# Kernel tuning notes

Measured on AMD Instinct MI355X. Metric: run time of the kernel, lower is better.

Reference implementation:

```python
import jax, jax.numpy as jnp
import numpy as np


def setup_inputs() -> dict:
    key = jax.random.key(0)
    ks = jax.random.split(key, 7)
    N, C, sy, sx = 1024, 384, 7, 7
    Dm, Dc = 64, 64
    Dg = C + Dm + Dc  # 512, must match f_t_global
    return {
        "f_t_global": jax.random.normal(ks[0], (N, Dg), dtype=jnp.float32),
        "x_t_local": jax.random.normal(ks[1], (N, C, sy, sx), dtype=jnp.float32),
        "x_t_prev_local": jax.random.normal(ks[2], (N, C, sy, sx), dtype=jnp.float32),
        "m_t": jax.random.normal(ks[3], (N, Dm), dtype=jnp.float32),
        "m_t_prev": jax.random.normal(ks[4], (N, Dm), dtype=jnp.float32),
        "c_t": jax.random.normal(ks[5], (N, Dc), dtype=jnp.float32),
        "c_t_prev": jax.random.normal(ks[6], (N, Dc), dtype=jnp.float32),
    }


def _join(loc, m, c):
    # loc: [S, N, C]; m: [N, Dm]; c: [N, Dc] -> [S, N, C+Dm+Dc]
    S, N, _ = loc.shape
    mc = jnp.concatenate([m, c], axis=-1)  # [N, Dm+Dc]
    mc = jnp.broadcast_to(mc[None], (S, N, mc.shape[-1]))
    return jnp.concatenate([loc, mc], axis=-1)


def _mean_ce_diag(logits):
    # logits: [S, N, N]; labels = arange(N) for every s -> mean over s of CE
    logp = jax.nn.log_softmax(logits, axis=-1)
    diag = jnp.diagonal(logp, axis1=1, axis2=2)  # [S, N]
    return -jnp.mean(diag)  # mean over N (per-step CE) and over S (the /(sx*sy))


def reference(f_t_global, x_t_local, x_t_prev_local, m_t, m_t_prev, c_t, c_t_prev):
    N, C, sy, sx = x_t_prev_local.shape
    S = sy * sx
    # [N,C,sy,sx] -> [S,N,C] (spatial locations batched)
    prev = x_t_prev_local.reshape(N, C, S).transpose(2, 0, 1)
    cur = x_t_local.reshape(N, C, S).transpose(2, 0, 1)
    pos = _join(prev, m_t_prev, c_t_prev)   # [S, N, D]
    # loss1: global features vs per-location previous positives
    logits1 = jnp.einsum('id,sjd->sij', f_t_global, pos)  # [S, N, N]
    loss1 = _mean_ce_diag(logits1)
    # loss2: per-location current predictions vs previous positives
    pred2 = _join(cur, m_t, c_t)            # [S, N, D]
    logits2 = jnp.einsum('sid,sjd->sij', pred2, pos)
    loss2 = _mean_ce_diag(logits2)
    loss = loss1 + loss2
    return (loss, x_t_prev_local, x_t_local)
```

## Files before the change

kernel.cpp:

```cpp
#include <hip/hip_runtime.h>
#include <hip/hip_bf16.h>

typedef __attribute__((ext_vector_type(8))) __bf16 bf16x8;
typedef __attribute__((ext_vector_type(4))) float  f32x4;

#define SDIM 49
#define NDIM 1024
#define CDIM 384
#define DDIM 512
#define DMC  64
#define SCALE (1.0f/(SDIM*NDIM))
#define SLOT4 32768
#define CHUNK 24576

__device__ __forceinline__ void gload16(const void* g, void* l) {
    __builtin_amdgcn_global_load_lds((const __attribute__((address_space(1))) void*)g,
                                     (__attribute__((address_space(3))) void*)l, 16, 0, 0);
}

__global__ __launch_bounds__(512) void front_kernel(
    const float* __restrict__ xp, const float* __restrict__ mp,
    const float* __restrict__ cp, __hip_bfloat16* __restrict__ Km,
    const float* __restrict__ x,  const float* __restrict__ mt,
    const float* __restrict__ ct, __hip_bfloat16* __restrict__ Qm,
    const float* __restrict__ f,  __hip_bfloat16* __restrict__ Fm,
    float* __restrict__ out0)
{
    const int bid = blockIdx.x;
    const int tid = threadIdx.x;

    if (tid < 256) {
        const int i = bid * 256 + tid;
        Fm[i] = __float2bfloat16(f[i]);
    }
    if (bid == 0 && tid == 0) out0[0] = 0.0f;

    const bool kside = (bid < 1024);
    const int j = kside ? bid : (bid - 1024);
    const float* xloc = kside ? xp : x;
    const float* mv   = kside ? mp : mt;
    const float* cv   = kside ? cp : ct;
    __hip_bfloat16* dst = kside ? Km : Qm;

    const int d = tid;
    float vals[SDIM];
    if (d < CDIM) {
        const float* p = xloc + ((size_t)j * CDIM + d) * SDIM;
        #pragma unroll
        for (int s = 0; s < SDIM; ++s) vals[s] = p[s];
    } else if (d < CDIM + DMC) {
        float v = mv[j * DMC + (d - CDIM)];
        #pragma unroll
        for (int s = 0; s < SDIM; ++s) vals[s] = v;
    } else {
        float v = cv[j * DMC + (d - CDIM - DMC)];
        #pragma unroll
        for (int s = 0; s < SDIM; ++s) vals[s] = v;
    }
    #pragma unroll
    for (int s = 0; s < SDIM; ++s)
        dst[((size_t)s * NDIM + j) * DDIM + d] = __float2bfloat16(vals[s]);
}

__global__ __launch_bounds__(512, 2) void loss_kernel(
    const __hip_bfloat16* __restrict__ Fm,
    const __hip_bfloat16* __restrict__ Km,
    const __hip_bfloat16* __restrict__ Qm,
    const float* __restrict__ xp,
    const float* __restrict__ xq,
    float* __restrict__ outv,
    float2* __restrict__ part,
    float* __restrict__ out)
{
    extern __shared__ __attribute__((aligned(16))) char sm[];

    const int bid = blockIdx.x;
    const int xcd = bid & 7;
    const int jj  = bid >> 3;
    const int g0  = 196 * xcd;
    const int gend = g0 + 196;

    const int tid  = threadIdx.x;
    const int lane = tid & 63;
    const int w    = tid >> 6;
    const int l15  = lane & 15;
    const int l4   = lane >> 4;
    const int wk   = w >> 2;
    const int wq   = w & 3;

    const int srow = tid >> 2;
    const int jcol = (((tid & 3) - ((tid >> 3) & 3)) & 3) << 4;

    const unsigned off   = (unsigned)(((l4 + (l15 >> 1)) & 3) << 4);
    const unsigned abase = (unsigned)((wk * 128 + l15) * 64);
    const unsigned bbase = 16384u + (unsigned)((wq * 64 + l15) * 64);

    auto APtr = [&](int g) -> const char* {
        const int s = g >> 5, kb = (g >> 3) & 3;
        return (const char*)Km + ((size_t)s * NDIM + (size_t)kb * 256) * 1024;
    };
    auto BPtr = [&](int g) -> const char* {
        const int s = g >> 5, qb = g & 7;
        return (qb < 4)
            ? ((const char*)Fm + (size_t)qb * 256 * 1024)
            : ((const char*)Qm + ((size_t)s * NDIM + (size_t)(qb - 4) * 256) * 1024);
    };
    auto stage4 = [&](const char* A, const char* B, int ko, char* slot) {
        #pragma unroll
        for (int c = 0; c < 2; ++c) {
            gload16(A + (size_t)(c * 128 + srow) * 1024 + ko + jcol,
                    slot + c * 8192 + tid * 16);
            gload16(B + (size_t)(c * 128 + srow) * 1024 + ko + jcol,
                    slot + 16384 + c * 8192 + tid * 16);
        }
    };

    f32x4 acc[8][4];
    bf16x8 afr[8], bfr[4];

    #define READ12() do {                                                     \
        _Pragma("unroll")                                                     \
        for (int a = 0; a < 8; ++a)                                           \
            afr[a] = *(const bf16x8*)(sb_ + abase + a * 1024u + off);         \
        _Pragma("unroll")                                                     \
        for (int b = 0; b < 4; ++b)                                           \
            bfr[b] = *(const bf16x8*)(sb_ + bbase + b * 1024u + off);         \
    } while (0)

    #define MFMA32() do {                                                     \
        _Pragma("unroll")                                                     \
        for (int a = 0; a < 8; ++a)                                           \
            _Pragma("unroll")                                                 \
            for (int b = 0; b < 4; ++b)                                       \
                acc[a][b] = __builtin_amdgcn_mfma_f32_16x16x32_bf16(          \
                    afr[a], bfr[b], acc[a][b], 0, 0, 0);                      \
    } while (0)

    {
        const char* A0 = APtr(g0 + jj);
        const char* B0 = BPtr(g0 + jj);
        stage4(A0, B0, 0,   sm);
        stage4(A0, B0, 64,  sm + SLOT4);
        stage4(A0, B0, 128, sm + 2 * SLOT4);
        asm volatile("s_waitcnt vmcnt(0)" ::: "memory");
    }

    for (int g = g0 + jj; g < gend; g += 32) {
        const char* Ag = APtr(g);
        const char* Bg = BPtr(g);
        const bool hasNext = (g + 32) < gend;
        const char* An = hasNext ? APtr(g + 32) : Ag;
        const char* Bn = hasNext ? BPtr(g + 32) : Bg;

        #pragma unroll
        for (int a = 0; a < 8; ++a)
            #pragma unroll
            for (int b = 0; b < 4; ++b) acc[a][b] = f32x4{0.f, 0.f, 0.f, 0.f};

        #pragma unroll
        for (int t = 0; t < 16; ++t) {
            const char* sb_ = sm + (size_t)(t & 3) * SLOT4;
            char* ns_ = sm + (size_t)((t + 3) & 3) * SLOT4;

            if (t == 15)      asm volatile("s_waitcnt vmcnt(0)" ::: "memory");
            else if (t == 14) asm volatile("s_waitcnt vmcnt(4)" ::: "memory");
            else if (t >= 3)  asm volatile("s_waitcnt vmcnt(8)" ::: "memory");
            __builtin_amdgcn_s_barrier();

            if (t <= 12) {
                stage4(Ag, Bg, (t + 3) * 64, ns_);
            } else if (hasNext) {
                stage4(An, Bn, (t - 13) * 64, ns_);
            }
            __builtin_amdgcn_sched_barrier(0);

            READ12();
            __builtin_amdgcn_s_setprio(1); MFMA32(); __builtin_amdgcn_s_setprio(0);
        }

        const int s  = g >> 5;
        const int kb = (g >> 3) & 3;
        const int qb = g & 7;

        const float* csrc = (g < 784) ? (xp + (size_t)g * CHUNK)
                                      : (xq + (size_t)(g - 784) * CHUNK);
        float* cdst = outv + (size_t)g * CHUNK;
        f32x4 cbuf[12];
        #pragma unroll
        for (int i = 0; i < 12; ++i)
            cbuf[i] = *(const f32x4*)(csrc + tid * 4 + i * 2048);

        float q_m[4], q_s[4];
        #pragma unroll
        for (int b = 0; b < 4; ++b) {
            float m = -3.0e38f;
            #pragma unroll
            for (int a = 0; a < 8; ++a)
                #pragma unroll
                for (int r = 0; r < 4; ++r) m = fmaxf(m, acc[a][b][r]);
            float ss = 0.0f;
            #pragma unroll
            for (int a = 0; a < 8; ++a)
                #pragma unroll
                for (int r = 0; r < 4; ++r) ss += __expf(acc[a][b][r] - m);
            #pragma unroll
            for (int off2 = 16; off2 <= 32; off2 <<= 1) {
                float mo = __shfl_xor(m, off2, 64);
                float so = __shfl_xor(ss, off2, 64);
                float nm = fmaxf(m, mo);
                ss = ss * __expf(m - nm) + so * __expf(mo - nm);
                m = nm;
            }
            q_m[b] = m; q_s[b] = ss;
        }

        if (kb == (qb & 3) && (wq >> 1) == wk) {
            float d = 0.0f;
            const bool lok = (((lane >> 2) & 3) == l4);
            if (wq & 1) {
                #pragma unroll
                for (int b = 0; b < 4; ++b)
                    #pragma unroll
                    for (int r = 0; r < 4; ++r)
                        if (lok && r == (lane & 3)) d += acc[4 + b][b][r];
            } else {
                #pragma unroll
                for (int b = 0; b < 4; ++b)
                    #pragma unroll
                    for (int r = 0; r < 4; ++r)
                        if (lok && r == (lane & 3)) d += acc[b][b][r];
            }
            #pragma unroll
            for (int off2 = 1; off2 < 64; off2 <<= 1) d += __shfl_xor(d, off2, 64);
            if (lane == 0) atomicAdd(out, -d * SCALE);
        }

        asm volatile("s_waitcnt vmcnt(0)" ::: "memory");
        #pragma unroll
        for (int i = 0; i < 12; ++i)
            *(f32x4*)(cdst + tid * 4 + i * 2048) = cbuf[i];

        if (lane < 16) {
            const size_t rowb = (size_t)s * 2048 + (size_t)qb * 256 + wq * 64 + lane;
            #pragma unroll
            for (int b = 0; b < 4; ++b)
                part[(rowb + b * 16) * 8 + kb * 2 + wk] = make_float2(q_m[b], q_s[b]);
        }
    }
    #undef READ12
    #undef MFMA32
}

__global__ __launch_bounds__(256) void reduce_kernel(
    const float2* __restrict__ part, float* __restrict__ out)
{
    const int row = blockIdx.x * 256 + threadIdx.x;
    const float2* p = part + (size_t)row * 8;
    float m = -3.0e38f;
    float2 q[8];
    #pragma unroll
    for (int i = 0; i < 8; ++i) { q[i] = p[i]; m = fmaxf(m, q[i].x); }
    float ssum = 0.0f;
    #pragma unroll
    for (int i = 0; i < 8; ++i) ssum += q[i].y * __expf(q[i].x - m);
    float v = m + __logf(ssum);
    #pragma unroll
    for (int off = 1; off < 64; off <<= 1) v += __shfl_xor(v, off, 64);
    __shared__ float red[4];
    const int lane = threadIdx.x & 63, w = threadIdx.x >> 6;
    if (lane == 0) red[w] = v;
    __syncthreads();
    if (threadIdx.x == 0)
        atomicAdd(out, (red[0] + red[1] + red[2] + red[3]) * SCALE);
}

extern "C" void kernel_launch(void* const* d_in, const int* in_sizes, int n_in,
                              void* d_out, int out_size, void* d_ws, size_t ws_size,
                              hipStream_t stream)
{
    (void)in_sizes; (void)n_in; (void)out_size; (void)ws_size;
    const float* f  = (const float*)d_in[0];
    const float* x  = (const float*)d_in[1];
    const float* xp = (const float*)d_in[2];
    const float* mt = (const float*)d_in[3];
    const float* mp = (const float*)d_in[4];
    const float* ct = (const float*)d_in[5];
    const float* cp = (const float*)d_in[6];
    float* out = (float*)d_out;

    char* ws = (char*)d_ws;
    const size_t packBytes = (size_t)SDIM * NDIM * DDIM * 2;
    __hip_bfloat16* Km = (__hip_bfloat16*)ws;
    __hip_bfloat16* Qm = (__hip_bfloat16*)(ws + packBytes);
    __hip_bfloat16* Fm = (__hip_bfloat16*)(ws + 2 * packBytes);
    float2* part = (float2*)(ws + 2 * packBytes + (size_t)NDIM * DDIM * 2);

    front_kernel<<<2048, 512, 0, stream>>>(xp, mp, cp, Km, x, mt, ct, Qm, f, Fm, out);
    loss_kernel<<<256, 512, 4 * SLOT4, stream>>>(Fm, Km, Qm, xp, x, out + 1, part, out);
    reduce_kernel<<<392, 256, 0, stream>>>(part, out);
}
```

Before: 208.7 us.

## Halve loss-kernel tile width, use triple-buffered LDS and double the grid

The loss GEMM tile shrinks from 256x256 to 256x128 per work item. Each block now stages A and B through three LDS slots instead of four, and the grid grows from 256 to 512 blocks with launch bounds asking for 4 blocks per CU. The partial softmax stats grow to 16 per row, and the reduce kernel is updated to merge them. The aim is higher occupancy and better latency hiding from smaller register and LDS footprints, at the cost of less data reuse per tile and more partial-stat traffic.

```diff
diff --git a/kernel.cpp b/kernel.cpp
--- a/kernel.cpp
+++ b/kernel.cpp
@@ -10,8 +10,8 @@
 #define DDIM 512
 #define DMC  64
 #define SCALE (1.0f/(SDIM*NDIM))
-#define SLOT4 32768
-#define CHUNK 24576
+#define SLOT3 24576
+#define CHUNK 12288
 
 __device__ __forceinline__ void gload16(const void* g, void* l) {
     __builtin_amdgcn_global_load_lds((const __attribute__((address_space(1))) void*)g,
@@ -62,7 +62,7 @@
         dst[((size_t)s * NDIM + j) * DDIM + d] = __float2bfloat16(vals[s]);
 }
 
-__global__ __launch_bounds__(512, 2) void loss_kernel(
+__global__ __launch_bounds__(512, 4) void loss_kernel(
     const __hip_bfloat16* __restrict__ Fm,
     const __hip_bfloat16* __restrict__ Km,
     const __hip_bfloat16* __restrict__ Qm,
@@ -77,117 +77,113 @@
     const int bid = blockIdx.x;
     const int xcd = bid & 7;
     const int jj  = bid >> 3;
-    const int g0  = 196 * xcd;
-    const int gend = g0 + 196;
 
     const int tid  = threadIdx.x;
     const int lane = tid & 63;
     const int w    = tid >> 6;
     const int l15  = lane & 15;
     const int l4   = lane >> 4;
-    const int wk   = w >> 2;
-    const int wq   = w & 3;
-
-    const int srow = tid >> 2;
+    const int wk   = w >> 1;
+    const int wq   = w & 1;
+
     const int jcol = (((tid & 3) - ((tid >> 3) & 3)) & 3) << 4;
 
     const unsigned off   = (unsigned)(((l4 + (l15 >> 1)) & 3) << 4);
-    const unsigned abase = (unsigned)((wk * 128 + l15) * 64);
+    const unsigned abase = (unsigned)((wk * 64 + l15) * 64);
     const unsigned bbase = 16384u + (unsigned)((wq * 64 + l15) * 64);
 
     auto APtr = [&](int g) -> const char* {
-        const int s = g >> 5, kb = (g >> 3) & 3;
+        const int s = g >> 6, kb = (g >> 4) & 3;
         return (const char*)Km + ((size_t)s * NDIM + (size_t)kb * 256) * 1024;
     };
     auto BPtr = [&](int g) -> const char* {
-        const int s = g >> 5, qb = g & 7;
-        return (qb < 4)
-            ? ((const char*)Fm + (size_t)qb * 256 * 1024)
-            : ((const char*)Qm + ((size_t)s * NDIM + (size_t)(qb - 4) * 256) * 1024);
+        const int s = g >> 6, qb = g & 15;
+        return (qb < 8)
+            ? ((const char*)Fm + (size_t)qb * 128 * 1024)
+            : ((const char*)Qm + ((size_t)s * NDIM + (size_t)(qb - 8) * 128) * 1024);
     };
-    auto stage4 = [&](const char* A, const char* B, int ko, char* slot) {
-        #pragma unroll
-        for (int c = 0; c < 2; ++c) {
-            gload16(A + (size_t)(c * 128 + srow) * 1024 + ko + jcol,
-                    slot + c * 8192 + tid * 16);
-            gload16(B + (size_t)(c * 128 + srow) * 1024 + ko + jcol,
-                    slot + 16384 + c * 8192 + tid * 16);
-        }
+    auto stage3 = [&](const char* A, const char* B, int ko, char* slot) {
+        const int r = tid >> 2;
+        gload16(A + (size_t)r * 1024 + ko + jcol,        slot + tid * 16);
+        gload16(A + (size_t)(128 + r) * 1024 + ko + jcol, slot + 8192 + tid * 16);
+        gload16(B + (size_t)r * 1024 + ko + jcol,        slot + 16384 + tid * 16);
     };
 
-    f32x4 acc[8][4];
-    bf16x8 afr[8], bfr[4];
-
-    #define READ12() do {                                                     \
+    f32x4 acc[4][4];
+    bf16x8 afr[4], bfr[4];
+
+    #define READ8() do {                                                      \
         _Pragma("unroll")                                                     \
-        for (int a = 0; a < 8; ++a)                                           \
+        for (int a = 0; a < 4; ++a)                                           \
             afr[a] = *(const bf16x8*)(sb_ + abase + a * 1024u + off);         \
         _Pragma("unroll")                                                     \
         for (int b = 0; b < 4; ++b)                                           \
             bfr[b] = *(const bf16x8*)(sb_ + bbase + b * 1024u + off);         \
     } while (0)
 
-    #define MFMA32() do {                                                     \
+    #define MFMA16() do {                                                     \
         _Pragma("unroll")                                                     \
-        for (int a = 0; a < 8; ++a)                                           \
+        for (int a = 0; a < 4; ++a)                                           \
             _Pragma("unroll")                                                 \
             for (int b = 0; b < 4; ++b)                                       \
                 acc[a][b] = __builtin_amdgcn_mfma_f32_16x16x32_bf16(          \
                     afr[a], bfr[b], acc[a][b], 0, 0, 0);                      \
     } while (0)
 
+    int cs = 0;
+
     {
-        const char* A0 = APtr(g0 + jj);
-        const char* B0 = BPtr(g0 + jj);
-        stage4(A0, B0, 0,   sm);
-        stage4(A0, B0, 64,  sm + SLOT4);
-        stage4(A0, B0, 128, sm + 2 * SLOT4);
-        asm volatile("s_waitcnt vmcnt(0)" ::: "memory");
-    }
-
-    for (int g = g0 + jj; g < gend; g += 32) {
+        const int gg = 392 * xcd + jj;
+        stage3(APtr(gg), BPtr(gg), 0,  sm);
+        stage3(APtr(gg), BPtr(gg), 64, sm + SLOT3);
+    }
+
+    for (int l = jj; l < 392; l += 64) {
+        const int g = 392 * xcd + l;
         const char* Ag = APtr(g);
         const char* Bg = BPtr(g);
-        const bool hasNext = (g + 32) < gend;
-        const char* An = hasNext ? APtr(g + 32) : Ag;
-        const char* Bn = hasNext ? BPtr(g + 32) : Bg;
-
-        #pragma unroll
-        for (int a = 0; a < 8; ++a)
+        const bool hasNext = (l + 64) < 392;
+        const int gn = hasNext ? (g + 64) : g;
+        const char* An = APtr(gn);
+        const char* Bn = BPtr(gn);
+
+        #pragma unroll
+        for (int a = 0; a < 4; ++a)
             #pragma unroll
             for (int b = 0; b < 4; ++b) acc[a][b] = f32x4{0.f, 0.f, 0.f, 0.f};
 
         #pragma unroll
         for (int t = 0; t < 16; ++t) {
-            const char* sb_ = sm + (size_t)(t & 3) * SLOT4;
-            char* ns_ = sm + (size_t)((t + 3) & 3) * SLOT4;
-
-            if (t == 15)      asm volatile("s_waitcnt vmcnt(0)" ::: "memory");
-            else if (t == 14) asm volatile("s_waitcnt vmcnt(4)" ::: "memory");
-            else if (t >= 3)  asm volatile("s_waitcnt vmcnt(8)" ::: "memory");
+            const char* sb_ = sm + (size_t)cs * SLOT3;
+            int ps = cs + 2; if (ps >= 3) ps -= 3;
+            char* ns_ = sm + (size_t)ps * SLOT3;
+
+            if (t == 15 && !hasNext) asm volatile("s_waitcnt vmcnt(0)" ::: "memory");
+            else                     asm volatile("s_waitcnt vmcnt(3)" ::: "memory");
             __builtin_amdgcn_s_barrier();
 
-            if (t <= 12) {
-                stage4(Ag, Bg, (t + 3) * 64, ns_);
+            if (t < 14) {
+                stage3(Ag, Bg, (t + 2) * 64, ns_);
             } else if (hasNext) {
-                stage4(An, Bn, (t - 13) * 64, ns_);
+                stage3(An, Bn, (t - 14) * 64, ns_);
             }
             __builtin_amdgcn_sched_barrier(0);
 
-            READ12();
-            __builtin_amdgcn_s_setprio(1); MFMA32(); __builtin_amdgcn_s_setprio(0);
-        }
-
-        const int s  = g >> 5;
-        const int kb = (g >> 3) & 3;
-        const int qb = g & 7;
-
-        const float* csrc = (g < 784) ? (xp + (size_t)g * CHUNK)
-                                      : (xq + (size_t)(g - 784) * CHUNK);
+            READ8();
+            __builtin_amdgcn_s_setprio(1); MFMA16(); __builtin_amdgcn_s_setprio(0);
+            cs = (cs == 2) ? 0 : cs + 1;
+        }
+
+        const int s  = g >> 6;
+        const int kb = (g >> 4) & 3;
+        const int qb = g & 15;
+
+        const float* csrc = (g < 1568) ? (xp + (size_t)g * CHUNK)
+                                       : (xq + (size_t)(g - 1568) * CHUNK);
         float* cdst = outv + (size_t)g * CHUNK;
-        f32x4 cbuf[12];
-        #pragma unroll
-        for (int i = 0; i < 12; ++i)
+        f32x4 cbuf[6];
+        #pragma unroll
+        for (int i = 0; i < 6; ++i)
             cbuf[i] = *(const f32x4*)(csrc + tid * 4 + i * 2048);
 
         float q_m[4], q_s[4];
@@ -195,12 +191,12 @@
         for (int b = 0; b < 4; ++b) {
             float m = -3.0e38f;
             #pragma unroll
-            for (int a = 0; a < 8; ++a)
+            for (int a = 0; a < 4; ++a)
                 #pragma unroll
                 for (int r = 0; r < 4; ++r) m = fmaxf(m, acc[a][b][r]);
             float ss = 0.0f;
             #pragma unroll
-            for (int a = 0; a < 8; ++a)
+            for (int a = 0; a < 4; ++a)
                 #pragma unroll
                 for (int r = 0; r < 4; ++r) ss += __expf(acc[a][b][r] - m);
             #pragma unroll
@@ -214,22 +210,14 @@
             q_m[b] = m; q_s[b] = ss;
         }
 
-        if (kb == (qb & 3) && (wq >> 1) == wk) {
+        if (kb == ((qb & 7) >> 1) && wk == ((qb & 7) & 1) * 2 + wq) {
             float d = 0.0f;
-            const bool lok = (((lane >> 2) & 3) == l4);
-            if (wq & 1) {
+            const bool lok = ((l15 >> 2) == l4);
+            #pragma unroll
+            for (int b = 0; b < 4; ++b)
                 #pragma unroll
-                for (int b = 0; b < 4; ++b)
-                    #pragma unroll
-                    for (int r = 0; r < 4; ++r)
-                        if (lok && r == (lane & 3)) d += acc[4 + b][b][r];
-            } else {
-                #pragma unroll
-                for (int b = 0; b < 4; ++b)
-                    #pragma unroll
-                    for (int r = 0; r < 4; ++r)
-                        if (lok && r == (lane & 3)) d += acc[b][b][r];
-            }
+                for (int r = 0; r < 4; ++r)
+                    if (lok && r == (lane & 3)) d += acc[b][b][r];
             #pragma unroll
             for (int off2 = 1; off2 < 64; off2 <<= 1) d += __shfl_xor(d, off2, 64);
             if (lane == 0) atomicAdd(out, -d * SCALE);
@@ -237,32 +225,33 @@
 
         asm volatile("s_waitcnt vmcnt(0)" ::: "memory");
         #pragma unroll
-        for (int i = 0; i < 12; ++i)
+        for (int i = 0; i < 6; ++i)
             *(f32x4*)(cdst + tid * 4 + i * 2048) = cbuf[i];
 
         if (lane < 16) {
-            const size_t rowb = (size_t)s * 2048 + (size_t)qb * 256 + wq * 64 + lane;
+            const size_t rowb = (size_t)s * 2048 + (size_t)(qb >= 8) * 1024
+                              + (size_t)(qb & 7) * 128 + wq * 64 + lane;
             #pragma unroll
             for (int b = 0; b < 4; ++b)
-                part[(rowb + b * 16) * 8 + kb * 2 + wk] = make_float2(q_m[b], q_s[b]);
-        }
-    }
-    #undef READ12
-    #undef MFMA32
+                part[(rowb + b * 16) * 16 + kb * 4 + wk] = make_float2(q_m[b], q_s[b]);
+        }
+    }
+    #undef READ8
+    #undef MFMA16
 }
 
 __global__ __launch_bounds__(256) void reduce_kernel(
     const float2* __restrict__ part, float* __restrict__ out)
 {
     const int row = blockIdx.x * 256 + threadIdx.x;
-    const float2* p = part + (size_t)row * 8;
+    const float2* p = part + (size_t)row * 16;
     float m = -3.0e38f;
-    float2 q[8];
-    #pragma unroll
-    for (int i = 0; i < 8; ++i) { q[i] = p[i]; m = fmaxf(m, q[i].x); }
+    float2 q[16];
+    #pragma unroll
+    for (int i = 0; i < 16; ++i) { q[i] = p[i]; m = fmaxf(m, q[i].x); }
     float ssum = 0.0f;
     #pragma unroll
-    for (int i = 0; i < 8; ++i) ssum += q[i].y * __expf(q[i].x - m);
+    for (int i = 0; i < 16; ++i) ssum += q[i].y * __expf(q[i].x - m);
     float v = m + __logf(ssum);
     #pragma unroll
     for (int off = 1; off < 64; off <<= 1) v += __shfl_xor(v, off, 64);
@@ -296,6 +285,6 @@
     float2* part = (float2*)(ws + 2 * packBytes + (size_t)NDIM * DDIM * 2);
 
     front_kernel<<<2048, 512, 0, stream>>>(xp, mp, cp, Km, x, mt, ct, Qm, f, Fm, out);
-    loss_kernel<<<256, 512, 4 * SLOT4, stream>>>(Fm, Km, Qm, xp, x, out + 1, part, out);
+    loss_kernel<<<512, 512, 3 * SLOT3, stream>>>(Fm, Km, Qm, xp, x, out + 1, part, out);
     reduce_kernel<<<392, 256, 0, stream>>>(part, out);
 }
```

After: 248.4 us. +19.1%, slower.
